# Performance work log

Hardware: AMD Instinct MI355X
Metric: run time of the kernel (lower is better)

Reference implementation:

```python
import jax, jax.numpy as jnp
import numpy as np

N_NODES = 100000
N_EDGES = 1600000
IN_CH = 128
HEADS = 4
OUT_CH = 32
NEG_SLOPE = 0.2
DIV_WEIGHT = 0.1
EPS_SOFTMAX = 1e-16  # PyG softmax eps
EPS_COS = 1e-8       # F.cosine_similarity eps


def setup_inputs() -> dict:
    key = jax.random.key(0)
    k1, k2, k3, k4, k5 = jax.random.split(key, 5)
    x = jax.random.normal(k1, (N_NODES, IN_CH), dtype=jnp.float32)
    # edge_index with guaranteed no self loops (remove_self_loops becomes a no-op)
    row = jax.random.randint(k2, (N_EDGES,), 0, N_NODES, dtype=jnp.int32)
    off = jax.random.randint(k3, (N_EDGES,), 1, N_NODES, dtype=jnp.int32)
    col = (row + off) % N_NODES
    edge_index = jnp.stack([row, col], axis=0)
    # params (xavier-ish scale)
    W = jax.random.normal(k4, (HEADS * OUT_CH, IN_CH), dtype=jnp.float32) * np.sqrt(2.0 / (IN_CH + HEADS * OUT_CH))
    att = jax.random.normal(k5, (1, HEADS, 2 * OUT_CH), dtype=jnp.float32) * np.sqrt(2.0 / (1 + 2 * OUT_CH))
    bias = jnp.zeros((HEADS * OUT_CH,), dtype=jnp.float32)
    return {"x": x, "edge_index": edge_index, "W": W, "att": att, "bias": bias}


def reference(x, edge_index, W, att, bias):
    N = x.shape[0]
    H = att.shape[1]
    C = att.shape[2] // 2
    idx_dtype = edge_index.dtype
    # add self loops (input has none, so remove_self_loops is a no-op)
    loops = jnp.arange(N, dtype=idx_dtype)
    row = jnp.concatenate([edge_index[0], loops])  # destination
    col = jnp.concatenate([edge_index[1], loops])  # source
    # linear projection -> [N, H, C]
    h = (x @ W.T).reshape(N, H, C)
    # attention logits: (cat(x_i, x_j) * att).sum(-1) == s_i[row] + s_j[col]
    s_i = jnp.einsum('nhc,hc->nh', h, att[0, :, :C])  # [N, H]
    s_j = jnp.einsum('nhc,hc->nh', h, att[0, :, C:])  # [N, H]
    e = s_i[row] + s_j[col]                            # [E, H]
    e = jnp.where(e >= 0, e, NEG_SLOPE * e)            # leaky_relu
    # segment softmax over destination node (row)
    e_max = jax.ops.segment_max(e, row, num_segments=N)
    e_max = jnp.where(jnp.isfinite(e_max), e_max, 0.0)
    e_exp = jnp.exp(e - e_max[row])
    denom = jax.ops.segment_sum(e_exp, row, num_segments=N)
    alpha = e_exp / (denom[row] + EPS_SOFTMAX)         # [E, H]
    # attention diversity loss: mean pairwise cosine sim (zero diagonal)
    gram = alpha.T @ alpha                             # [H, H]
    norms = jnp.sqrt(jnp.diag(gram))
    corr = gram / jnp.maximum(norms[:, None] * norms[None, :], EPS_COS)
    corr = corr * (1.0 - jnp.eye(H, dtype=corr.dtype))
    diversity_loss = jnp.mean(corr) * DIV_WEIGHT
    # weighted message + scatter-add aggregation (dropout p=0 -> identity)
    msg = h[col] * alpha[:, :, None]                   # [E, H, C]
    out = jax.ops.segment_sum(msg, row, num_segments=N)
    out = out.reshape(N, H * C) + bias                 # concat=True
    return out, diversity_loss
```

## Files before the change

kernel.cpp:

```cpp
#include <hip/hip_runtime.h>
#include <math.h>

#define HC     128
#define SLOT   64
#define AGG_BLOCKS 2048
#define PREP_GRID  2048
#define NPART  8

typedef unsigned int uint32;
typedef unsigned long long uint64;
typedef short bf16x8 __attribute__((ext_vector_type(8)));
typedef float f32x4 __attribute__((ext_vector_type(4)));

__device__ inline unsigned short f2bf(float f){
  uint32 u = __float_as_uint(f);
  u = (u + 0x7fffu + ((u >> 16) & 1u)) >> 16;
  return (unsigned short)u;
}
__device__ inline uint32 pack_bf2(float a, float b){
  return (uint32)f2bf(a) | ((uint32)f2bf(b) << 16);
}
__device__ inline void lds_fence(){
  asm volatile("s_waitcnt lgkmcnt(0)" ::: "memory");
  __builtin_amdgcn_sched_barrier(0);
}


__global__ __launch_bounds__(256) void k_prep(const float* __restrict__ x, const float* __restrict__ W,
                                              const float* __restrict__ att,
                                              const int* __restrict__ row, const int* __restrict__ col,
                                              int* cnt, int* bucket,
                                              uint32* __restrict__ h_pair,
                                              float* __restrict__ s_i, float* __restrict__ s_j,
                                              int N, int E, int ntiles){
  __shared__ __align__(16) unsigned short Blds[128*128];
  int t = threadIdx.x;
  bool hasTile = ((int)blockIdx.x < ntiles);

  if (hasTile){
    int w = t >> 6, l = t & 63;
    int o = l & 15, lg = l >> 4;
    int n0 = blockIdx.x * 64;

    #pragma unroll
    for (int i = 0; i < 8; ++i){
      int id = t + i*256;
      int r  = id >> 4, ck = id & 15;
      int sw = ck ^ (r & 7);
      float4 b0 = *(const float4*)&W[(size_t)r*128 + ck*8];
      float4 b1 = *(const float4*)&W[(size_t)r*128 + ck*8 + 4];
      bf16x8 pb;
      pb[0]=(short)f2bf(b0.x); pb[1]=(short)f2bf(b0.y); pb[2]=(short)f2bf(b0.z); pb[3]=(short)f2bf(b0.w);
      pb[4]=(short)f2bf(b1.x); pb[5]=(short)f2bf(b1.y); pb[6]=(short)f2bf(b1.z); pb[7]=(short)f2bf(b1.w);
      *(bf16x8*)&Blds[r*128 + sw*8] = pb;
    }

    int arow = n0 + w*16 + o;
    bool rok = (arow < N);
    const float* xr = x + (size_t)arow*128;
    bf16x8 afr[4];
    #pragma unroll
    for (int ks = 0; ks < 4; ++ks){
      float4 a0 = make_float4(0.f,0.f,0.f,0.f), a1 = a0;
      if (rok){
        a0 = *(const float4*)&xr[ks*32 + lg*8];
        a1 = *(const float4*)&xr[ks*32 + lg*8 + 4];
      }
      bf16x8 pa;
      pa[0]=(short)f2bf(a0.x); pa[1]=(short)f2bf(a0.y); pa[2]=(short)f2bf(a0.z); pa[3]=(short)f2bf(a0.w);
      pa[4]=(short)f2bf(a1.x); pa[5]=(short)f2bf(a1.y); pa[6]=(short)f2bf(a1.z); pa[7]=(short)f2bf(a1.w);
      afr[ks] = pa;
    }
    __syncthreads();

    f32x4 acc[8];
    #pragma unroll
    for (int cf = 0; cf < 8; ++cf) acc[cf] = (f32x4){0.f,0.f,0.f,0.f};

    #pragma unroll
    for (int ks = 0; ks < 4; ++ks){
      int ckk = ks*4 + lg;
      #pragma unroll
      for (int cf = 0; cf < 8; ++cf){
        int rb = cf*16 + o;
        bf16x8 bfr = *(const bf16x8*)&Blds[rb*128 + (ckk ^ (rb & 7))*8];
        acc[cf] = __builtin_amdgcn_mfma_f32_16x16x32_bf16(afr[ks], bfr, acc[cf], 0, 0, 0);
      }
    }

    float ai0[4], ai1[4], aj0[4], aj1[4];
    #pragma unroll
    for (int hd = 0; hd < 4; ++hd){
      ai0[hd] = att[hd*64 + o];
      ai1[hd] = att[hd*64 + 16 + o];
      aj0[hd] = att[hd*64 + 32 + o];
      aj1[hd] = att[hd*64 + 48 + o];
    }

    #pragma unroll
    for (int q = 0; q < 4; ++q){
      int node = n0 + w*16 + lg*4 + q;
      float v[8];
      #pragma unroll
      for (int cf = 0; cf < 8; ++cf) v[cf] = acc[cf][q];
      float pi[4], pj[4];
      #pragma unroll
      for (int hd = 0; hd < 4; ++hd){
        pi[hd] = v[2*hd]*ai0[hd] + v[2*hd+1]*ai1[hd];
        pj[hd] = v[2*hd]*aj0[hd] + v[2*hd+1]*aj1[hd];
      }
      #pragma unroll
      for (int sh = 1; sh < 16; sh <<= 1){
        #pragma unroll
        for (int hd = 0; hd < 4; ++hd){
          pi[hd] += __shfl_xor(pi[hd], sh);
          pj[hd] += __shfl_xor(pj[hd], sh);
        }
      }
      if (node < N){
        #pragma unroll
        for (int hd = 0; hd < 4; ++hd)
          h_pair[(size_t)node*64 + hd*16 + o] = pack_bf2(v[2*hd], v[2*hd+1]);
        if (o == 0){
          *(float4*)&s_i[(size_t)node*4] = make_float4(pi[0], pi[1], pi[2], pi[3]);
          *(float4*)&s_j[(size_t)node*4] = make_float4(pj[0], pj[1], pj[2], pj[3]);
        }
      }
    }
  }

  {
    int k = blockIdx.x & (NPART-1);
    int c = blockIdx.x >> 3;
    int CH = PREP_GRID / NPART;
    int per  = (E + CH - 1) / CH;
    int base = c * per;
    int end  = base + per; if (end > E) end = E;
    int rng  = (N + NPART - 1) / NPART;
    int lo = k * rng, hi = lo + rng;
    for (int i = base + t; i < end; i += 256){
      int d = row[i];
      if (d >= lo && d < hi){
        int pos = atomicAdd(&cnt[d], 1);
        if (pos < SLOT-1) bucket[(size_t)d*SLOT + pos] = col[i];
      }
    }
  }
}


__global__ __launch_bounds__(256) void k_agg(const uint32* __restrict__ h_pair, const float* __restrict__ s_i,
                                             const float* __restrict__ s_j, const int* __restrict__ cnt,
                                             const int* __restrict__ bucket,
                                             const float* __restrict__ bias, float* __restrict__ out,
                                             float* __restrict__ gram_part, int N){
  __shared__ __align__(16) float al[4][SLOT*4];
  __shared__ int   cs[4][SLOT];
  __shared__ float red[4][10];
  const uint2* hp2 = (const uint2*)h_pair;
  int t = threadIdx.x;
  int w = t >> 6, l = t & 63;
  int g = l >> 4, o = l & 15;
  int lw = l & 31, half = l >> 5;
  int g2 = lw >> 3;
  int o0 = (2*lw) & 15;
  int cbase = 32*g2 + (half << 4) + o0;
  float2 bv = *(const float2*)&bias[cbase];
  float ga[10];
  #pragma unroll
  for (int p = 0; p < 10; ++p) ga[p] = 0.f;
  int TW = gridDim.x * 4;

  for (int n = blockIdx.x*4 + w; n < N; n += TW){
    int dc = cnt[n]; if (dc > SLOT-1) dc = SLOT-1;
    int d  = dc + 1;
    float4 si = *(const float4*)&s_i[(size_t)n*4];
    if (l < d){
      int src = (l < dc) ? __builtin_nontemporal_load(&bucket[(size_t)n*SLOT + l]) : n;
      cs[w][l] = src << 5;
      float4 sj = *(const float4*)&s_j[(size_t)src*4];
      float4 e;
      e.x = si.x + sj.x; e.y = si.y + sj.y; e.z = si.z + sj.z; e.w = si.w + sj.w;
      e.x = e.x >= 0.f ? e.x : 0.2f*e.x;
      e.y = e.y >= 0.f ? e.y : 0.2f*e.y;
      e.z = e.z >= 0.f ? e.z : 0.2f*e.z;
      e.w = e.w >= 0.f ? e.w : 0.2f*e.w;
      *(float4*)&al[w][l*4] = e;
    }
    if ((d & 1) && l == d){
      cs[w][l] = n << 5;
      *(float4*)&al[w][l*4] = make_float4(0.f,0.f,0.f,0.f);
    }
    lds_fence();
    float m = -3.4e38f;
    for (int j = o; j < d; j += 16) m = fmaxf(m, al[w][j*4 + g]);
    #pragma unroll
    for (int sh = 1; sh < 16; sh <<= 1) m = fmaxf(m, __shfl_xor(m, sh));
    float sum = 0.f;
    for (int j = o; j < d; j += 16){
      float v = __expf(al[w][j*4 + g] - m);
      al[w][j*4 + g] = v;
      sum += v;
    }
    #pragma unroll
    for (int sh = 1; sh < 16; sh <<= 1) sum += __shfl_xor(sum, sh);
    float r = 1.f/(sum + 1e-16f);
    for (int j = o; j < d; j += 16) al[w][j*4 + g] *= r;
    lds_fence();
    if (l < d){
      float4 a = *(const float4*)&al[w][l*4];
      ga[0] += a.x*a.x; ga[1] += a.x*a.y; ga[2] += a.x*a.z; ga[3] += a.x*a.w;
      ga[4] += a.y*a.y; ga[5] += a.y*a.z; ga[6] += a.y*a.w;
      ga[7] += a.z*a.z; ga[8] += a.z*a.w;
      ga[9] += a.w*a.w;
    }
    float a0 = 0.f, a1 = 0.f, a2 = 0.f, a3 = 0.f;
    const float* alw = &al[w][0];
    const int*   csw = &cs[w][0];
    int npair = (d + 1) >> 1;
    int i = 0;
    for (; i + 4 <= npair; i += 4){
      int e0 = 2*i + half, e1 = e0 + 2, e2 = e0 + 4, e3 = e0 + 6;
      int s0 = csw[e0], s1 = csw[e1], s2 = csw[e2], s3 = csw[e3];
      float w0 = alw[e0*4 + g2], w1 = alw[e1*4 + g2];
      float w2 = alw[e2*4 + g2], w3 = alw[e3*4 + g2];
      uint2 v0 = hp2[(size_t)(uint32)(s0 + lw)];
      uint2 v1 = hp2[(size_t)(uint32)(s1 + lw)];
      uint2 v2 = hp2[(size_t)(uint32)(s2 + lw)];
      uint2 v3 = hp2[(size_t)(uint32)(s3 + lw)];
      a0 += w0 * __uint_as_float(v0.x << 16);  a1 += w0 * __uint_as_float(v0.x & 0xffff0000u);
      a2 += w0 * __uint_as_float(v0.y << 16);  a3 += w0 * __uint_as_float(v0.y & 0xffff0000u);
      a0 += w1 * __uint_as_float(v1.x << 16);  a1 += w1 * __uint_as_float(v1.x & 0xffff0000u);
      a2 += w1 * __uint_as_float(v1.y << 16);  a3 += w1 * __uint_as_float(v1.y & 0xffff0000u);
      a0 += w2 * __uint_as_float(v2.x << 16);  a1 += w2 * __uint_as_float(v2.x & 0xffff0000u);
      a2 += w2 * __uint_as_float(v2.y << 16);  a3 += w2 * __uint_as_float(v2.y & 0xffff0000u);
      a0 += w3 * __uint_as_float(v3.x << 16);  a1 += w3 * __uint_as_float(v3.x & 0xffff0000u);
      a2 += w3 * __uint_as_float(v3.y << 16);  a3 += w3 * __uint_as_float(v3.y & 0xffff0000u);
    }
    for (; i < npair; ++i){
      int e = 2*i + half;
      float aw = alw[e*4 + g2];
      uint2 v = hp2[(size_t)(uint32)(csw[e] + lw)];
      a0 += aw * __uint_as_float(v.x << 16);  a1 += aw * __uint_as_float(v.x & 0xffff0000u);
      a2 += aw * __uint_as_float(v.y << 16);  a3 += aw * __uint_as_float(v.y & 0xffff0000u);
    }
    a0 += __shfl_xor(a0, 32);
    a1 += __shfl_xor(a1, 32);
    a2 += __shfl_xor(a2, 32);
    a3 += __shfl_xor(a3, 32);
    union { float f[2]; uint64 u; } st;
    st.f[0] = (half ? a1 : a0) + bv.x;
    st.f[1] = (half ? a3 : a2) + bv.y;
    __builtin_nontemporal_store(st.u, (uint64*)&out[(size_t)n*128 + cbase]);
    lds_fence();
  }
  __syncthreads();
  #pragma unroll
  for (int p = 0; p < 10; ++p){
    float v = ga[p];
    #pragma unroll
    for (int sh = 1; sh < 64; sh <<= 1) v += __shfl_xor(v, sh);
    ga[p] = v;
  }
  if (l == 0){
    #pragma unroll
    for (int p = 0; p < 10; ++p) red[w][p] = ga[p];
  }
  __syncthreads();
  if (t == 0){
    #pragma unroll
    for (int p = 0; p < 10; ++p)
      gram_part[(size_t)blockIdx.x*10 + p] = red[0][p] + red[1][p] + red[2][p] + red[3][p];
  }
}


__global__ __launch_bounds__(256) void k_final(const float* __restrict__ gram_part, int nparts,
                                               float* __restrict__ loss){
  __shared__ float red[4][10];
  int t = threadIdx.x;
  float acc[10];
  #pragma unroll
  for (int p = 0; p < 10; ++p) acc[p] = 0.f;
  for (int i = t; i < nparts; i += 256){
    #pragma unroll
    for (int p = 0; p < 10; ++p) acc[p] += gram_part[(size_t)i*10 + p];
  }
  #pragma unroll
  for (int p = 0; p < 10; ++p){
    float v = acc[p];
    #pragma unroll
    for (int sh = 1; sh < 64; sh <<= 1) v += __shfl_xor(v, sh);
    acc[p] = v;
  }
  if ((t & 63) == 0){
    #pragma unroll
    for (int p = 0; p < 10; ++p) red[t >> 6][p] = acc[p];
  }
  __syncthreads();
  if (t == 0){
    float gs[10];
    #pragma unroll
    for (int p = 0; p < 10; ++p) gs[p] = red[0][p] + red[1][p] + red[2][p] + red[3][p];
    float G[4][4];
    G[0][0]=gs[0]; G[0][1]=gs[1]; G[0][2]=gs[2]; G[0][3]=gs[3];
    G[1][0]=gs[1]; G[1][1]=gs[4]; G[1][2]=gs[5]; G[1][3]=gs[6];
    G[2][0]=gs[2]; G[2][1]=gs[5]; G[2][2]=gs[7]; G[2][3]=gs[8];
    G[3][0]=gs[3]; G[3][1]=gs[6]; G[3][2]=gs[8]; G[3][3]=gs[9];
    float nr[4];
    for (int i = 0; i < 4; ++i) nr[i] = sqrtf(G[i][i]);
    float ssum = 0.f;
    for (int i = 0; i < 4; ++i)
      for (int j = 0; j < 4; ++j)
        if (i != j) ssum += G[i][j] / fmaxf(nr[i]*nr[j], 1e-8f);
    loss[0] = ssum * (0.1f/16.f);
  }
}


extern "C" void kernel_launch(void* const* d_in, const int* in_sizes, int n_in,
                              void* d_out, int out_size, void* d_ws, size_t ws_size,
                              hipStream_t stream){
  const float* x    = (const float*)d_in[0];
  const int*   edge = (const int*)d_in[1];
  const float* W    = (const float*)d_in[2];
  const float* att  = (const float*)d_in[3];
  const float* bias = (const float*)d_in[4];
  int N = in_sizes[0] / 128;
  int E = in_sizes[1] / 2;
  const int* row = edge;
  const int* col = edge + E;
  float* out  = (float*)d_out;
  float* loss = out + (size_t)N*HC;

  char* wsb = (char*)d_ws;
  size_t off = 0;
  auto alloc = [&](size_t bytes)->void*{
    size_t o = (off + 255) & ~(size_t)255;
    off = o + bytes;
    return (void*)(wsb + o);
  };
  uint32* h_pair   = (uint32*)alloc((size_t)N*64*sizeof(uint32));
  float* s_i       = (float*)alloc((size_t)N*4*sizeof(float));
  float* s_j       = (float*)alloc((size_t)N*4*sizeof(float));
  int*   cnt       = (int*)alloc((size_t)N*sizeof(int));
  int*   bucket    = (int*)alloc((size_t)N*SLOT*sizeof(int));
  float* gram_part = (float*)alloc((size_t)AGG_BLOCKS*10*sizeof(float));
  (void)ws_size; (void)n_in; (void)out_size;

  hipMemsetAsync(cnt, 0, (size_t)N*sizeof(int), stream);
  int ntiles = (N+63)/64;
  k_prep<<<PREP_GRID,256,0,stream>>>(x, W, att, row, col, cnt, bucket, h_pair, s_i, s_j, N, E, ntiles);
  k_agg<<<AGG_BLOCKS,256,0,stream>>>(h_pair, s_i, s_j, cnt, bucket, bias, out, gram_part, N);
  k_final<<<1,256,0,stream>>>(gram_part, AGG_BLOCKS, loss);
}
```

Measured before the change: 207.4 us.

## Pre-convert W to bf16 once, read B fragments from global, fuse cnt zeroing

Adds a small init kernel that converts W to bf16 once and zeroes the counters, replacing the hipMemsetAsync. k_prep no longer stages W into a 32KB LDS tile with a block barrier; each wave reads its bf16 B fragments straight from global/L2. This removes the per-block W conversion, the LDS traffic and the syncthreads, and frees LDS for higher occupancy, at the cost of more global/L2 loads. Nontemporal loads and stores are also applied to x reads and to the h_pair/s_i/s_j writes.

```diff
diff --git a/kernel.cpp b/kernel.cpp
--- a/kernel.cpp
+++ b/kernel.cpp
@@ -26,14 +26,24 @@
 }
 
 
-__global__ __launch_bounds__(256) void k_prep(const float* __restrict__ x, const float* __restrict__ W,
+__global__ __launch_bounds__(256) void k_init(const float* __restrict__ W, unsigned short* __restrict__ W_bf,
+                                              int* cnt, int N){
+  int gid = blockIdx.x*256 + threadIdx.x;
+  if (gid < 8192){
+    float2 v = *(const float2*)&W[2*gid];
+    *(uint32*)&W_bf[2*gid] = pack_bf2(v.x, v.y);
+  }
+  for (int i = gid; i < N; i += gridDim.x*256) cnt[i] = 0;
+}
+
+
+__global__ __launch_bounds__(256) void k_prep(const float* __restrict__ x, const unsigned short* __restrict__ W_bf,
                                               const float* __restrict__ att,
                                               const int* __restrict__ row, const int* __restrict__ col,
                                               int* cnt, int* bucket,
                                               uint32* __restrict__ h_pair,
                                               float* __restrict__ s_i, float* __restrict__ s_j,
                                               int N, int E, int ntiles){
-  __shared__ __align__(16) unsigned short Blds[128*128];
   int t = threadIdx.x;
   bool hasTile = ((int)blockIdx.x < ntiles);
 
@@ -42,36 +52,22 @@
     int o = l & 15, lg = l >> 4;
     int n0 = blockIdx.x * 64;
 
-    #pragma unroll
-    for (int i = 0; i < 8; ++i){
-      int id = t + i*256;
-      int r  = id >> 4, ck = id & 15;
-      int sw = ck ^ (r & 7);
-      float4 b0 = *(const float4*)&W[(size_t)r*128 + ck*8];
-      float4 b1 = *(const float4*)&W[(size_t)r*128 + ck*8 + 4];
-      bf16x8 pb;
-      pb[0]=(short)f2bf(b0.x); pb[1]=(short)f2bf(b0.y); pb[2]=(short)f2bf(b0.z); pb[3]=(short)f2bf(b0.w);
-      pb[4]=(short)f2bf(b1.x); pb[5]=(short)f2bf(b1.y); pb[6]=(short)f2bf(b1.z); pb[7]=(short)f2bf(b1.w);
-      *(bf16x8*)&Blds[r*128 + sw*8] = pb;
-    }
-
     int arow = n0 + w*16 + o;
     bool rok = (arow < N);
     const float* xr = x + (size_t)arow*128;
     bf16x8 afr[4];
     #pragma unroll
     for (int ks = 0; ks < 4; ++ks){
-      float4 a0 = make_float4(0.f,0.f,0.f,0.f), a1 = a0;
+      f32x4 a0 = (f32x4){0.f,0.f,0.f,0.f}, a1 = a0;
       if (rok){
-        a0 = *(const float4*)&xr[ks*32 + lg*8];
-        a1 = *(const float4*)&xr[ks*32 + lg*8 + 4];
+        a0 = __builtin_nontemporal_load((const f32x4*)&xr[ks*32 + lg*8]);
+        a1 = __builtin_nontemporal_load((const f32x4*)&xr[ks*32 + lg*8 + 4]);
       }
       bf16x8 pa;
-      pa[0]=(short)f2bf(a0.x); pa[1]=(short)f2bf(a0.y); pa[2]=(short)f2bf(a0.z); pa[3]=(short)f2bf(a0.w);
-      pa[4]=(short)f2bf(a1.x); pa[5]=(short)f2bf(a1.y); pa[6]=(short)f2bf(a1.z); pa[7]=(short)f2bf(a1.w);
+      pa[0]=(short)f2bf(a0[0]); pa[1]=(short)f2bf(a0[1]); pa[2]=(short)f2bf(a0[2]); pa[3]=(short)f2bf(a0[3]);
+      pa[4]=(short)f2bf(a1[0]); pa[5]=(short)f2bf(a1[1]); pa[6]=(short)f2bf(a1[2]); pa[7]=(short)f2bf(a1[3]);
       afr[ks] = pa;
     }
-    __syncthreads();
 
     f32x4 acc[8];
     #pragma unroll
@@ -79,11 +75,10 @@
 
     #pragma unroll
     for (int ks = 0; ks < 4; ++ks){
-      int ckk = ks*4 + lg;
       #pragma unroll
       for (int cf = 0; cf < 8; ++cf){
         int rb = cf*16 + o;
-        bf16x8 bfr = *(const bf16x8*)&Blds[rb*128 + (ckk ^ (rb & 7))*8];
+        bf16x8 bfr = *(const bf16x8*)&W_bf[(size_t)rb*128 + ks*32 + lg*8];
         acc[cf] = __builtin_amdgcn_mfma_f32_16x16x32_bf16(afr[ks], bfr, acc[cf], 0, 0, 0);
       }
     }
@@ -120,10 +115,13 @@
       if (node < N){
         #pragma unroll
         for (int hd = 0; hd < 4; ++hd)
-          h_pair[(size_t)node*64 + hd*16 + o] = pack_bf2(v[2*hd], v[2*hd+1]);
+          __builtin_nontemporal_store(pack_bf2(v[2*hd], v[2*hd+1]),
+                                      &h_pair[(size_t)node*64 + hd*16 + o]);
         if (o == 0){
-          *(float4*)&s_i[(size_t)node*4] = make_float4(pi[0], pi[1], pi[2], pi[3]);
-          *(float4*)&s_j[(size_t)node*4] = make_float4(pj[0], pj[1], pj[2], pj[3]);
+          f32x4 vi = (f32x4){pi[0], pi[1], pi[2], pi[3]};
+          f32x4 vj = (f32x4){pj[0], pj[1], pj[2], pj[3]};
+          __builtin_nontemporal_store(vi, (f32x4*)&s_i[(size_t)node*4]);
+          __builtin_nontemporal_store(vj, (f32x4*)&s_j[(size_t)node*4]);
         }
       }
     }
@@ -345,12 +343,13 @@
   float* s_j       = (float*)alloc((size_t)N*4*sizeof(float));
   int*   cnt       = (int*)alloc((size_t)N*sizeof(int));
   int*   bucket    = (int*)alloc((size_t)N*SLOT*sizeof(int));
+  unsigned short* W_bf = (unsigned short*)alloc(16384*sizeof(unsigned short));
   float* gram_part = (float*)alloc((size_t)AGG_BLOCKS*10*sizeof(float));
   (void)ws_size; (void)n_in; (void)out_size;
 
-  hipMemsetAsync(cnt, 0, (size_t)N*sizeof(int), stream);
+  k_init<<<128,256,0,stream>>>(W, W_bf, cnt, N);
   int ntiles = (N+63)/64;
-  k_prep<<<PREP_GRID,256,0,stream>>>(x, W, att, row, col, cnt, bucket, h_pair, s_i, s_j, N, E, ntiles);
+  k_prep<<<PREP_GRID,256,0,stream>>>(x, W_bf, att, row, col, cnt, bucket, h_pair, s_i, s_j, N, E, ntiles);
   k_agg<<<AGG_BLOCKS,256,0,stream>>>(h_pair, s_i, s_j, cnt, bucket, bias, out, gram_part, N);
   k_final<<<1,256,0,stream>>>(gram_part, AGG_BLOCKS, loss);
 }
```

Result: slower. 228.9 us (+10.4%).
